# Performance work log

Hardware: AMD Instinct MI355X
Metric: run time of the kernel (lower is better)

Reference implementation:

```python
import jax, jax.numpy as jnp
import numpy as np

ALPHA_BASE = 1.2
ALPHA_SCALE = 0.3
GRAPH_LAMBDA = 0.3
FUSION_BETA = 0.1
PRIOR_BETA = 0.2
LN_EPS = 1e-5  # nn.LayerNorm default

B, L, C = 8, 8192, 512
STAT, HID, GF, EMB = 4, 16, 16, 16


def _linear_params(key, out_d, in_d):
    kw, kb = jax.random.split(key)
    bound = 1.0 / np.sqrt(in_d)
    W = jax.random.uniform(kw, (out_d, in_d), minval=-bound, maxval=bound, dtype=jnp.float32)
    b = jax.random.uniform(kb, (out_d,), minval=-bound, maxval=bound, dtype=jnp.float32)
    return W, b


def setup_inputs() -> dict:
    key = jax.random.key(0)
    ks = jax.random.split(key, 9)
    residual = jax.random.normal(ks[0], (B, L, C), dtype=jnp.float32)
    node_embedding = jax.random.normal(ks[1], (C, EMB), dtype=jnp.float32) * 0.02
    W_l1, b_l1 = _linear_params(ks[2], HID, STAT)
    W_l2, b_l2 = _linear_params(ks[3], HID, HID)
    W_g, b_g = _linear_params(ks[4], HID, STAT)
    W_q, b_q = _linear_params(ks[5], GF, STAT)
    W_k, b_k = _linear_params(ks[6], GF, STAT)
    W_f, b_f = _linear_params(ks[7], HID, HID)
    W_o, b_o = _linear_params(ks[8], 1, HID)
    ln_g = jnp.ones((HID,), jnp.float32)
    ln_b = jnp.zeros((HID,), jnp.float32)
    return dict(residual=residual, node_embedding=node_embedding,
                W_l1=W_l1, b_l1=b_l1, W_l2=W_l2, b_l2=b_l2,
                W_g=W_g, b_g=b_g, W_q=W_q, b_q=b_q, W_k=W_k, b_k=b_k,
                W_f=W_f, b_f=b_f, W_o=W_o, b_o=b_o, ln_g=ln_g, ln_b=ln_b)


def reference(residual, node_embedding, W_l1, b_l1, W_l2, b_l2, W_g, b_g,
              W_q, b_q, W_k, b_k, W_f, b_f, W_o, b_o, ln_g, ln_b):
    # --- residual statistics: [B,L,C] -> [B,C,4] ---
    abs_res = jnp.abs(residual)
    m = abs_res.mean(axis=1)                       # mean(|r|)
    mx = abs_res.max(axis=1)                       # max(|r|)
    sq = (residual * residual).mean(axis=1)        # energy == mean(|r|^2)
    std = jnp.sqrt(jnp.maximum(sq - m * m, 0.0))   # biased std of |r|
    h0 = jnp.stack([m, mx, std, sq], axis=-1)      # [B,C,4]

    # --- local branch ---
    h_local = jax.nn.relu(h0 @ W_l1.T + b_l1) @ W_l2.T + b_l2  # [B,C,H]

    # --- adaptive adjacency ---
    q = h0 @ W_q.T + b_q                            # [B,C,G]
    k = h0 @ W_k.T + b_k                            # [B,C,G]
    sim_data = jax.nn.relu(jnp.einsum('bcg,bdg->bcd', q, k))
    sim_prior = jax.nn.relu(node_embedding @ node_embedding.T)  # [C,C]
    eye = jnp.eye(sim_data.shape[-1], dtype=sim_data.dtype)
    sim = sim_data + PRIOR_BETA * sim_prior[None] + eye[None]
    A = jax.nn.softmax(sim, axis=-1)                # [B,C,C]

    # --- message passing ---
    h_graph_in = h0 @ W_g.T + b_g                   # [B,C,H]
    msg = jnp.einsum('bcd,bdh->bch', A, h_graph_in)
    h_graph = h_graph_in + GRAPH_LAMBDA * jax.nn.relu(msg)

    # --- fusion + layernorm + head ---
    h = h_local + FUSION_BETA * h_graph
    mu = h.mean(axis=-1, keepdims=True)
    var = ((h - mu) ** 2).mean(axis=-1, keepdims=True)
    h = (h - mu) / jnp.sqrt(var + LN_EPS) * ln_g + ln_b
    h = jax.nn.relu(h @ W_f.T + b_f)
    delta = ALPHA_SCALE * jnp.tanh(h @ W_o.T + b_o)  # [B,C,1]
    alpha = (ALPHA_BASE + delta).transpose(0, 2, 1)  # [B,1,C]
    return alpha, h0, A
```

## Files before the change

### kernel.cpp

```cpp
#include <hip/hip_runtime.h>
#include <math.h>

#define BB 8
#define LL 8192
#define CC 512
#define NCHUNK 256

#define H0_OFF (BB*CC)
#define A_OFF  (H0_OFF + BB*CC*4)

#define F_ALPHA_BASE 1.2f
#define F_ALPHA_SCALE 0.3f
#define F_GRAPH_LAMBDA 0.3f
#define F_FUSION_BETA 0.1f
#define F_PRIOR_BETA 0.2f
#define F_LN_EPS 1e-5f

__global__ __launch_bounds__(256) void k_stats(const float* __restrict__ res,
                                               float* __restrict__ pbuf) {
    int b = blockIdx.x >> 8;
    int cb = blockIdx.x & 255;
    int c2 = threadIdx.x * 2;
    const float* base = res + ((size_t)b * LL + (size_t)cb * 32) * CC + c2;

    float s0 = 0.f, s1 = 0.f, m0 = 0.f, m1 = 0.f, q0 = 0.f, q1 = 0.f;
    #pragma unroll 8
    for (int r = 0; r < 32; r++) {
        float2 v = *(const float2*)(base + (size_t)r * CC);
        s0 += fabsf(v.x); s1 += fabsf(v.y);
        m0 = fmaxf(m0, fabsf(v.x)); m1 = fmaxf(m1, fabsf(v.y));
        q0 = fmaf(v.x, v.x, q0); q1 = fmaf(v.y, v.y, q1);
    }
    float* pb = pbuf + (size_t)((b * NCHUNK + cb) * 3) * CC + c2;
    *(float2*)(pb)          = make_float2(s0, s1);
    *(float2*)(pb + CC)     = make_float2(m0, m1);
    *(float2*)(pb + 2 * CC) = make_float2(q0, q1);
}

__global__ __launch_bounds__(256) void k_mid(const float* __restrict__ pbuf,
                                             const float* __restrict__ ne,
                                             float* __restrict__ prior,
                                             float* __restrict__ out) {
    if (blockIdx.x < 64) {
        __shared__ float red[4][3][64];
        int lane = threadIdx.x & 63;
        int part = threadIdx.x >> 6;
        int g = blockIdx.x * 64 + lane;
        int b = g >> 9;
        int c = g & 511;
        float sum = 0.f, mx = 0.f, sq = 0.f;
        const float* p = pbuf + (size_t)((b * NCHUNK + part * 64) * 3) * CC + c;
        #pragma unroll 8
        for (int ch = 0; ch < 64; ch++) {
            sum += p[0];
            mx = fmaxf(mx, p[CC]);
            sq += p[2 * CC];
            p += 3 * CC;
        }
        red[part][0][lane] = sum;
        red[part][1][lane] = mx;
        red[part][2][lane] = sq;
        __syncthreads();
        if (threadIdx.x < 64) {
            float ts = red[0][0][lane] + red[1][0][lane] + red[2][0][lane] + red[3][0][lane];
            float tm = fmaxf(fmaxf(red[0][1][lane], red[1][1][lane]),
                             fmaxf(red[2][1][lane], red[3][1][lane]));
            float tq = red[0][2][lane] + red[1][2][lane] + red[2][2][lane] + red[3][2][lane];
            float m = ts * (1.f / LL);
            float sqm = tq * (1.f / LL);
            float sd = sqrtf(fmaxf(sqm - m * m, 0.f));
            *(float4*)(out + H0_OFF + (size_t)g * 4) = make_float4(m, tm, sd, sqm);
        }
    } else {
        int idx = (blockIdx.x - 64) * 256 + threadIdx.x;
        int c = idx >> 9;
        int d = idx & 511;
        float s = 0.f;
        #pragma unroll
        for (int t = 0; t < 16; t++) s = fmaf(ne[c * 16 + t], ne[d * 16 + t], s);
        prior[idx] = fmaxf(s, 0.f);
    }
}

__global__ __launch_bounds__(256) void k_rows(
    const float* __restrict__ h0,
    const float* __restrict__ prior,
    const float* __restrict__ Wl1, const float* __restrict__ bl1,
    const float* __restrict__ Wl2, const float* __restrict__ bl2,
    const float* __restrict__ Wg,  const float* __restrict__ bg,
    const float* __restrict__ Wq,  const float* __restrict__ bq,
    const float* __restrict__ Wk,  const float* __restrict__ bk,
    const float* __restrict__ Wf,  const float* __restrict__ bf,
    const float* __restrict__ Wo,  const float* __restrict__ bo,
    const float* __restrict__ lng, const float* __restrict__ lnb,
    float* __restrict__ out) {
    __shared__ float kls[8 * CC * 2];
    __shared__ float hgls[8 * CC * 2];
    int b = blockIdx.x >> 6;
    int rb = blockIdx.x & 63;

    #pragma unroll
    for (int ccy = 0; ccy < 2; ccy++) {
        int col = threadIdx.x + ccy * 256;
        float4 hv = *(const float4*)(h0 + ((size_t)b * CC + col) * 4);
        float s[4] = {hv.x, hv.y, hv.z, hv.w};
        #pragma unroll
        for (int t2 = 0; t2 < 8; t2++) {
            float k0 = bk[2 * t2], k1 = bk[2 * t2 + 1];
            float g0 = bg[2 * t2], g1 = bg[2 * t2 + 1];
            #pragma unroll
            for (int j = 0; j < 4; j++) {
                k0 = fmaf(Wk[(2 * t2) * 4 + j], s[j], k0);
                k1 = fmaf(Wk[(2 * t2 + 1) * 4 + j], s[j], k1);
                g0 = fmaf(Wg[(2 * t2) * 4 + j], s[j], g0);
                g1 = fmaf(Wg[(2 * t2 + 1) * 4 + j], s[j], g1);
            }
            *(float2*)&kls[(t2 * CC + col) * 2] = make_float2(k0, k1);
            *(float2*)&hgls[(t2 * CC + col) * 2] = make_float2(g0, g1);
        }
    }
    __syncthreads();

    int wid = threadIdx.x >> 6;
    int lane = threadIdx.x & 63;
    int row0 = rb * 8 + wid * 2;

    float s2[2][4];
    float qr[2][16];
    #pragma unroll
    for (int rr = 0; rr < 2; rr++) {
        float4 hr = *(const float4*)(h0 + ((size_t)b * CC + row0 + rr) * 4);
        s2[rr][0] = hr.x; s2[rr][1] = hr.y; s2[rr][2] = hr.z; s2[rr][3] = hr.w;
        #pragma unroll
        for (int i = 0; i < 16; i++) {
            float a = bq[i];
            #pragma unroll
            for (int j = 0; j < 4; j++) a = fmaf(Wq[i * 4 + j], s2[rr][j], a);
            qr[rr][i] = a;
        }
    }

    const float* prow0 = prior + (size_t)row0 * CC;
    float sv[2][8];
    float mx0 = -1e30f, mx1 = -1e30f;
    #pragma unroll
    for (int j = 0; j < 8; j++) {
        int col = lane + 64 * j;
        float a0 = 0.f, a1 = 0.f;
        #pragma unroll
        for (int t2 = 0; t2 < 8; t2++) {
            float2 kk = *(const float2*)&kls[(t2 * CC + col) * 2];
            a0 = fmaf(qr[0][2 * t2], kk.x, a0);
            a0 = fmaf(qr[0][2 * t2 + 1], kk.y, a0);
            a1 = fmaf(qr[1][2 * t2], kk.x, a1);
            a1 = fmaf(qr[1][2 * t2 + 1], kk.y, a1);
        }
        float p0 = prow0[col], p1 = prow0[CC + col];
        float v0 = fmaxf(a0, 0.f) + F_PRIOR_BETA * p0 + (col == row0 ? 1.f : 0.f);
        float v1 = fmaxf(a1, 0.f) + F_PRIOR_BETA * p1 + (col == row0 + 1 ? 1.f : 0.f);
        sv[0][j] = v0; sv[1][j] = v1;
        mx0 = fmaxf(mx0, v0); mx1 = fmaxf(mx1, v1);
    }
    #pragma unroll
    for (int o = 32; o; o >>= 1) {
        mx0 = fmaxf(mx0, __shfl_xor(mx0, o));
        mx1 = fmaxf(mx1, __shfl_xor(mx1, o));
    }

    float ls0 = 0.f, ls1 = 0.f;
    float msg[2][16];
    #pragma unroll
    for (int h = 0; h < 16; h++) { msg[0][h] = 0.f; msg[1][h] = 0.f; }
    #pragma unroll
    for (int j = 0; j < 8; j++) {
        int col = lane + 64 * j;
        float e0 = expf(sv[0][j] - mx0);
        float e1 = expf(sv[1][j] - mx1);
        sv[0][j] = e0; sv[1][j] = e1;
        ls0 += e0; ls1 += e1;
        #pragma unroll
        for (int t2 = 0; t2 < 8; t2++) {
            float2 hh = *(const float2*)&hgls[(t2 * CC + col) * 2];
            msg[0][2 * t2]     = fmaf(e0, hh.x, msg[0][2 * t2]);
            msg[0][2 * t2 + 1] = fmaf(e0, hh.y, msg[0][2 * t2 + 1]);
            msg[1][2 * t2]     = fmaf(e1, hh.x, msg[1][2 * t2]);
            msg[1][2 * t2 + 1] = fmaf(e1, hh.y, msg[1][2 * t2 + 1]);
        }
    }
    #pragma unroll
    for (int o = 32; o; o >>= 1) {
        ls0 += __shfl_xor(ls0, o);
        ls1 += __shfl_xor(ls1, o);
    }
    float inv0 = 1.f / ls0, inv1 = 1.f / ls1;

    float* arow0 = out + A_OFF + ((size_t)b * CC + row0) * CC;
    #pragma unroll
    for (int j = 0; j < 8; j++) {
        arow0[lane + 64 * j]      = sv[0][j] * inv0;
        arow0[CC + lane + 64 * j] = sv[1][j] * inv1;
    }

    #pragma unroll
    for (int h = 0; h < 16; h++) {
        float v0 = msg[0][h], v1 = msg[1][h];
        #pragma unroll
        for (int o = 32; o; o >>= 1) {
            v0 += __shfl_xor(v0, o);
            v1 += __shfl_xor(v1, o);
        }
        msg[0][h] = v0 * inv0;
        msg[1][h] = v1 * inv1;
    }

    #pragma unroll
    for (int rr = 0; rr < 2; rr++) {
        int row = row0 + rr;
        float t1[16];
        #pragma unroll
        for (int i = 0; i < 16; i++) {
            float a = bl1[i];
            #pragma unroll
            for (int j = 0; j < 4; j++) a = fmaf(Wl1[i * 4 + j], s2[rr][j], a);
            t1[i] = fmaxf(a, 0.f);
        }
        float hvec[16];
        float mu = 0.f;
        #pragma unroll
        for (int h = 0; h < 16; h++) {
            float hl = bl2[h];
            #pragma unroll
            for (int j = 0; j < 16; j++) hl = fmaf(Wl2[h * 16 + j], t1[j], hl);
            float hgr = hgls[((h >> 1) * CC + row) * 2 + (h & 1)];
            float hg2 = hgr + F_GRAPH_LAMBDA * fmaxf(msg[rr][h], 0.f);
            float hv = hl + F_FUSION_BETA * hg2;
            hvec[h] = hv;
            mu += hv;
        }
        mu *= (1.f / 16.f);
        float var = 0.f;
        #pragma unroll
        for (int h = 0; h < 16; h++) { float d = hvec[h] - mu; var = fmaf(d, d, var); }
        var *= (1.f / 16.f);
        float istd = 1.f / sqrtf(var + F_LN_EPS);
        float hn[16];
        #pragma unroll
        for (int h = 0; h < 16; h++) hn[h] = (hvec[h] - mu) * istd * lng[h] + lnb[h];

        float acc2 = bo[0];
        #pragma unroll
        for (int o = 0; o < 16; o++) {
            float f = bf[o];
            #pragma unroll
            for (int t = 0; t < 16; t++) f = fmaf(Wf[o * 16 + t], hn[t], f);
            acc2 = fmaf(Wo[o], fmaxf(f, 0.f), acc2);
        }
        float alpha = F_ALPHA_BASE + F_ALPHA_SCALE * tanhf(acc2);
        if (lane == 0) out[(size_t)b * CC + row] = alpha;
    }
}

extern "C" void kernel_launch(void* const* d_in, const int* in_sizes, int n_in,
                              void* d_out, int out_size, void* d_ws, size_t ws_size,
                              hipStream_t stream) {
    const float* res = (const float*)d_in[0];
    const float* ne  = (const float*)d_in[1];
    const float* Wl1 = (const float*)d_in[2];
    const float* bl1 = (const float*)d_in[3];
    const float* Wl2 = (const float*)d_in[4];
    const float* bl2 = (const float*)d_in[5];
    const float* Wg  = (const float*)d_in[6];
    const float* bg  = (const float*)d_in[7];
    const float* Wq  = (const float*)d_in[8];
    const float* bq  = (const float*)d_in[9];
    const float* Wk  = (const float*)d_in[10];
    const float* bk  = (const float*)d_in[11];
    const float* Wf  = (const float*)d_in[12];
    const float* bf  = (const float*)d_in[13];
    const float* Wo  = (const float*)d_in[14];
    const float* bo  = (const float*)d_in[15];
    const float* lng = (const float*)d_in[16];
    const float* lnb = (const float*)d_in[17];
    float* out = (float*)d_out;
    float* ws  = (float*)d_ws;

    float* pbuf = ws;
    float* prior = ws + (size_t)BB * NCHUNK * 3 * CC;

    k_stats<<<BB * NCHUNK, 256, 0, stream>>>(res, pbuf);
    k_mid<<<64 + (CC * CC) / 256, 256, 0, stream>>>(pbuf, ne, prior, out);
    k_rows<<<BB * (CC / 8), 256, 0, stream>>>(out + H0_OFF, prior,
                                              Wl1, bl1, Wl2, bl2, Wg, bg, Wq, bq, Wk, bk,
                                              Wf, bf, Wo, bo, lng, lnb, out);
}
```

Before: 55.98 us.

## Fuse prior computation into row kernel and restructure stats reduction

The stats kernel now uses float4 loads with two half-blocks that combine their partials through shared memory, and it writes partials in a [b][stat][chunk][c] layout. The mid kernel is replaced by a lighter reduction kernel that spreads work over more blocks and finishes with shuffles. The node-embedding prior is no longer materialised as a CxC buffer in global memory; k_rows recomputes each needed prior entry from the embeddings. This removes a 1 MB write and read plus part of a launch, at the cost of redundant prior FMAs in every batch block.

```diff
diff --git a/kernel.cpp b/kernel.cpp
--- a/kernel.cpp
+++ b/kernel.cpp
@@ -18,73 +18,91 @@
 
 __global__ __launch_bounds__(256) void k_stats(const float* __restrict__ res,
                                                float* __restrict__ pbuf) {
+    __shared__ float comb[3][CC];
     int b = blockIdx.x >> 8;
     int cb = blockIdx.x & 255;
-    int c2 = threadIdx.x * 2;
-    const float* base = res + ((size_t)b * LL + (size_t)cb * 32) * CC + c2;
-
-    float s0 = 0.f, s1 = 0.f, m0 = 0.f, m1 = 0.f, q0 = 0.f, q1 = 0.f;
-    #pragma unroll 8
-    for (int r = 0; r < 32; r++) {
-        float2 v = *(const float2*)(base + (size_t)r * CC);
-        s0 += fabsf(v.x); s1 += fabsf(v.y);
+    int sub = threadIdx.x >> 7;
+    int c4 = (threadIdx.x & 127) * 4;
+    const float* base = res + ((size_t)b * LL + (size_t)cb * 32 + sub * 16) * CC + c4;
+
+    float s0 = 0.f, s1 = 0.f, s2 = 0.f, s3 = 0.f;
+    float m0 = 0.f, m1 = 0.f, m2 = 0.f, m3 = 0.f;
+    float q0 = 0.f, q1 = 0.f, q2 = 0.f, q3 = 0.f;
+    #pragma unroll
+    for (int r = 0; r < 16; r++) {
+        float4 v = *(const float4*)(base + (size_t)r * CC);
+        s0 += fabsf(v.x); s1 += fabsf(v.y); s2 += fabsf(v.z); s3 += fabsf(v.w);
         m0 = fmaxf(m0, fabsf(v.x)); m1 = fmaxf(m1, fabsf(v.y));
+        m2 = fmaxf(m2, fabsf(v.z)); m3 = fmaxf(m3, fabsf(v.w));
         q0 = fmaf(v.x, v.x, q0); q1 = fmaf(v.y, v.y, q1);
-    }
-    float* pb = pbuf + (size_t)((b * NCHUNK + cb) * 3) * CC + c2;
-    *(float2*)(pb)          = make_float2(s0, s1);
-    *(float2*)(pb + CC)     = make_float2(m0, m1);
-    *(float2*)(pb + 2 * CC) = make_float2(q0, q1);
+        q2 = fmaf(v.z, v.z, q2); q3 = fmaf(v.w, v.w, q3);
+    }
+    if (sub == 1) {
+        *(float4*)&comb[0][c4] = make_float4(s0, s1, s2, s3);
+        *(float4*)&comb[1][c4] = make_float4(m0, m1, m2, m3);
+        *(float4*)&comb[2][c4] = make_float4(q0, q1, q2, q3);
+    }
+    __syncthreads();
+    if (sub == 0) {
+        float4 cs = *(const float4*)&comb[0][c4];
+        float4 cm = *(const float4*)&comb[1][c4];
+        float4 cq = *(const float4*)&comb[2][c4];
+        s0 += cs.x; s1 += cs.y; s2 += cs.z; s3 += cs.w;
+        m0 = fmaxf(m0, cm.x); m1 = fmaxf(m1, cm.y);
+        m2 = fmaxf(m2, cm.z); m3 = fmaxf(m3, cm.w);
+        q0 += cq.x; q1 += cq.y; q2 += cq.z; q3 += cq.w;
+        float* pb = pbuf + ((size_t)(b * 3) * NCHUNK + cb) * CC + c4;
+        *(float4*)(pb)                        = make_float4(s0, s1, s2, s3);
+        *(float4*)(pb + (size_t)NCHUNK * CC)     = make_float4(m0, m1, m2, m3);
+        *(float4*)(pb + (size_t)2 * NCHUNK * CC) = make_float4(q0, q1, q2, q3);
+    }
 }
 
-__global__ __launch_bounds__(256) void k_mid(const float* __restrict__ pbuf,
-                                             const float* __restrict__ ne,
-                                             float* __restrict__ prior,
+__global__ __launch_bounds__(256) void k_red(const float* __restrict__ pbuf,
                                              float* __restrict__ out) {
-    if (blockIdx.x < 64) {
-        __shared__ float red[4][3][64];
-        int lane = threadIdx.x & 63;
-        int part = threadIdx.x >> 6;
-        int g = blockIdx.x * 64 + lane;
-        int b = g >> 9;
-        int c = g & 511;
-        float sum = 0.f, mx = 0.f, sq = 0.f;
-        const float* p = pbuf + (size_t)((b * NCHUNK + part * 64) * 3) * CC + c;
-        #pragma unroll 8
-        for (int ch = 0; ch < 64; ch++) {
-            sum += p[0];
-            mx = fmaxf(mx, p[CC]);
-            sq += p[2 * CC];
-            p += 3 * CC;
-        }
-        red[part][0][lane] = sum;
-        red[part][1][lane] = mx;
-        red[part][2][lane] = sq;
-        __syncthreads();
-        if (threadIdx.x < 64) {
-            float ts = red[0][0][lane] + red[1][0][lane] + red[2][0][lane] + red[3][0][lane];
-            float tm = fmaxf(fmaxf(red[0][1][lane], red[1][1][lane]),
-                             fmaxf(red[2][1][lane], red[3][1][lane]));
-            float tq = red[0][2][lane] + red[1][2][lane] + red[2][2][lane] + red[3][2][lane];
-            float m = ts * (1.f / LL);
-            float sqm = tq * (1.f / LL);
-            float sd = sqrtf(fmaxf(sqm - m * m, 0.f));
-            *(float4*)(out + H0_OFF + (size_t)g * 4) = make_float4(m, tm, sd, sqm);
-        }
-    } else {
-        int idx = (blockIdx.x - 64) * 256 + threadIdx.x;
-        int c = idx >> 9;
-        int d = idx & 511;
-        float s = 0.f;
-        #pragma unroll
-        for (int t = 0; t < 16; t++) s = fmaf(ne[c * 16 + t], ne[d * 16 + t], s);
-        prior[idx] = fmaxf(s, 0.f);
+    __shared__ float red[4][3][16];
+    int b = blockIdx.x >> 5;
+    int c16g = blockIdx.x & 31;
+    int coff = threadIdx.x & 15;
+    int part = threadIdx.x >> 4;
+    int c = c16g * 16 + coff;
+
+    const float* pA = pbuf + ((size_t)(b * 3 + 0) * NCHUNK + part * 16) * CC + c;
+    const float* pB = pbuf + ((size_t)(b * 3 + 1) * NCHUNK + part * 16) * CC + c;
+    const float* pC = pbuf + ((size_t)(b * 3 + 2) * NCHUNK + part * 16) * CC + c;
+    float sum = 0.f, mx = 0.f, sq = 0.f;
+    #pragma unroll
+    for (int i = 0; i < 16; i++) {
+        sum += pA[(size_t)i * CC];
+        mx = fmaxf(mx, pB[(size_t)i * CC]);
+        sq += pC[(size_t)i * CC];
+    }
+    sum += __shfl_xor(sum, 16); sum += __shfl_xor(sum, 32);
+    mx = fmaxf(mx, __shfl_xor(mx, 16)); mx = fmaxf(mx, __shfl_xor(mx, 32));
+    sq += __shfl_xor(sq, 16); sq += __shfl_xor(sq, 32);
+    int w = threadIdx.x >> 6;
+    if ((threadIdx.x & 63) < 16) {
+        red[w][0][coff] = sum;
+        red[w][1][coff] = mx;
+        red[w][2][coff] = sq;
+    }
+    __syncthreads();
+    if (threadIdx.x < 16) {
+        float ts = red[0][0][coff] + red[1][0][coff] + red[2][0][coff] + red[3][0][coff];
+        float tm = fmaxf(fmaxf(red[0][1][coff], red[1][1][coff]),
+                         fmaxf(red[2][1][coff], red[3][1][coff]));
+        float tq = red[0][2][coff] + red[1][2][coff] + red[2][2][coff] + red[3][2][coff];
+        float m = ts * (1.f / LL);
+        float sqm = tq * (1.f / LL);
+        float sd = sqrtf(fmaxf(sqm - m * m, 0.f));
+        int g = b * CC + c16g * 16 + coff;
+        *(float4*)(out + H0_OFF + (size_t)g * 4) = make_float4(m, tm, sd, sqm);
     }
 }
 
 __global__ __launch_bounds__(256) void k_rows(
     const float* __restrict__ h0,
-    const float* __restrict__ prior,
+    const float* __restrict__ ne,
     const float* __restrict__ Wl1, const float* __restrict__ bl1,
     const float* __restrict__ Wl2, const float* __restrict__ bl2,
     const float* __restrict__ Wg,  const float* __restrict__ bg,
@@ -98,6 +116,36 @@
     __shared__ float hgls[8 * CC * 2];
     int b = blockIdx.x >> 6;
     int rb = blockIdx.x & 63;
+    int wid = threadIdx.x >> 6;
+    int lane = threadIdx.x & 63;
+    int row0 = rb * 8 + wid * 2;
+
+    float nr[2][16];
+    #pragma unroll
+    for (int rr = 0; rr < 2; rr++) {
+        #pragma unroll
+        for (int t = 0; t < 4; t++) {
+            float4 v = *(const float4*)(ne + (size_t)(row0 + rr) * 16 + t * 4);
+            nr[rr][4 * t] = v.x; nr[rr][4 * t + 1] = v.y;
+            nr[rr][4 * t + 2] = v.z; nr[rr][4 * t + 3] = v.w;
+        }
+    }
+    float pr[2][8];
+    #pragma unroll
+    for (int j = 0; j < 8; j++) {
+        int col = lane + 64 * j;
+        float d0 = 0.f, d1 = 0.f;
+        #pragma unroll
+        for (int t = 0; t < 4; t++) {
+            float4 v = *(const float4*)(ne + (size_t)col * 16 + t * 4);
+            d0 = fmaf(nr[0][4 * t], v.x, d0); d0 = fmaf(nr[0][4 * t + 1], v.y, d0);
+            d0 = fmaf(nr[0][4 * t + 2], v.z, d0); d0 = fmaf(nr[0][4 * t + 3], v.w, d0);
+            d1 = fmaf(nr[1][4 * t], v.x, d1); d1 = fmaf(nr[1][4 * t + 1], v.y, d1);
+            d1 = fmaf(nr[1][4 * t + 2], v.z, d1); d1 = fmaf(nr[1][4 * t + 3], v.w, d1);
+        }
+        pr[0][j] = fmaxf(d0, 0.f);
+        pr[1][j] = fmaxf(d1, 0.f);
+    }
 
     #pragma unroll
     for (int ccy = 0; ccy < 2; ccy++) {
@@ -121,10 +169,6 @@
     }
     __syncthreads();
 
-    int wid = threadIdx.x >> 6;
-    int lane = threadIdx.x & 63;
-    int row0 = rb * 8 + wid * 2;
-
     float s2[2][4];
     float qr[2][16];
     #pragma unroll
@@ -140,7 +184,6 @@
         }
     }
 
-    const float* prow0 = prior + (size_t)row0 * CC;
     float sv[2][8];
     float mx0 = -1e30f, mx1 = -1e30f;
     #pragma unroll
@@ -155,9 +198,8 @@
             a1 = fmaf(qr[1][2 * t2], kk.x, a1);
             a1 = fmaf(qr[1][2 * t2 + 1], kk.y, a1);
         }
-        float p0 = prow0[col], p1 = prow0[CC + col];
-        float v0 = fmaxf(a0, 0.f) + F_PRIOR_BETA * p0 + (col == row0 ? 1.f : 0.f);
-        float v1 = fmaxf(a1, 0.f) + F_PRIOR_BETA * p1 + (col == row0 + 1 ? 1.f : 0.f);
+        float v0 = fmaxf(a0, 0.f) + F_PRIOR_BETA * pr[0][j] + (col == row0 ? 1.f : 0.f);
+        float v1 = fmaxf(a1, 0.f) + F_PRIOR_BETA * pr[1][j] + (col == row0 + 1 ? 1.f : 0.f);
         sv[0][j] = v0; sv[1][j] = v1;
         mx0 = fmaxf(mx0, v0); mx1 = fmaxf(mx1, v1);
     }
@@ -282,14 +324,11 @@
     const float* lng = (const float*)d_in[16];
     const float* lnb = (const float*)d_in[17];
     float* out = (float*)d_out;
-    float* ws  = (float*)d_ws;
-
-    float* pbuf = ws;
-    float* prior = ws + (size_t)BB * NCHUNK * 3 * CC;
+    float* pbuf = (float*)d_ws;
 
     k_stats<<<BB * NCHUNK, 256, 0, stream>>>(res, pbuf);
-    k_mid<<<64 + (CC * CC) / 256, 256, 0, stream>>>(pbuf, ne, prior, out);
-    k_rows<<<BB * (CC / 8), 256, 0, stream>>>(out + H0_OFF, prior,
+    k_red<<<BB * 32, 256, 0, stream>>>(pbuf, out);
+    k_rows<<<BB * (CC / 8), 256, 0, stream>>>(out + H0_OFF, ne,
                                               Wl1, bl1, Wl2, bl2, Wg, bg, Wq, bq, Wk, bk,
                                               Wf, bf, Wo, bo, lng, lnb, out);
 }
```

After: 58.20 us. +4.0%, slower.
